# Performance work log

Hardware: AMD Instinct MI355X
Metric: run time of the kernel (lower is better)

The kernel has to match this reference:

```python
import jax, jax.numpy as jnp
import numpy as np

N_NODES = 50000
NEG_SLOPE = 0.2


def gat_conv(x, src, dst, W, att_src, att_dst, bias, concat):
    # x: [N, F_in], W: [H*D, F_in], att_*: [H, D], bias: [H*D] or [D]
    N = x.shape[0]
    H, D = att_src.shape
    h = (x @ W.T).reshape(N, H, D)                      # [N, H, D]
    a_src = jnp.einsum('nhd,hd->nh', h, att_src)        # [N, H]
    a_dst = jnp.einsum('nhd,hd->nh', h, att_dst)        # [N, H]
    e = jax.nn.leaky_relu(a_src[src] + a_dst[dst], NEG_SLOPE)  # [E, H]
    # softmax over incoming edges of each destination node
    m = jax.ops.segment_max(e, dst, num_segments=N)     # [N, H]
    ex = jnp.exp(e - m[dst])
    denom = jax.ops.segment_sum(ex, dst, num_segments=N)
    alpha = ex / denom[dst]                             # [E, H]
    msg = alpha[:, :, None] * h[src]                    # [E, H, D]
    out = jax.ops.segment_sum(msg, dst, num_segments=N) # [N, H, D]
    out = out.reshape(N, H * D) if concat else out.mean(axis=1)
    return out + bias


def setup_inputs() -> dict:
    key = jax.random.key(0)
    ks = jax.random.split(key, 10)
    nfeat, nhid, nclass, heads = 256, 128, 40, 4
    d1 = nhid // heads  # 32
    E = 800000
    x = jax.random.normal(ks[0], (N_NODES, nfeat), dtype=jnp.float32)
    edge_index = jax.random.randint(ks[1], (2, E), 0, N_NODES, dtype=jnp.int64)
    s = 0.1
    W1 = jax.random.normal(ks[2], (heads * d1, nfeat), dtype=jnp.float32) * s
    att_src1 = jax.random.normal(ks[3], (heads, d1), dtype=jnp.float32) * s
    att_dst1 = jax.random.normal(ks[4], (heads, d1), dtype=jnp.float32) * s
    b1 = jnp.zeros((heads * d1,), dtype=jnp.float32)
    W2 = jax.random.normal(ks[5], (nclass, nhid), dtype=jnp.float32) * s
    att_src2 = jax.random.normal(ks[6], (1, nclass), dtype=jnp.float32) * s
    att_dst2 = jax.random.normal(ks[7], (1, nclass), dtype=jnp.float32) * s
    b2 = jnp.zeros((nclass,), dtype=jnp.float32)
    return {"x": x, "edge_index": edge_index, "W1": W1, "att_src1": att_src1,
            "att_dst1": att_dst1, "b1": b1, "W2": W2, "att_src2": att_src2,
            "att_dst2": att_dst2, "b2": b2}


def reference(x, edge_index, W1, att_src1, att_dst1, b1, W2, att_src2, att_dst2, b2):
    # PyG GATConv adds self-loops by default
    loops = jnp.arange(N_NODES, dtype=edge_index.dtype)
    src = jnp.concatenate([edge_index[0], loops])
    dst = jnp.concatenate([edge_index[1], loops])
    h = gat_conv(x, src, dst, W1, att_src1, att_dst1, b1, concat=True)
    h = jax.nn.relu(h)
    # dropout is identity in eval mode
    out = gat_conv(h, src, dst, W2, att_src2, att_dst2, b2, concat=True)
    return out
```

## Files before the change

kernel.cpp:

```cpp
#include <hip/hip_runtime.h>
#include <hip/hip_bf16.h>
#include <cstdint>
#include <cstddef>

#define N_NODES 50000
#define NEG_SLOPE 0.2f
#define NB 196
#define BIN_CHUNK 8192
#define SLICE_MAX 14336

typedef float floatx4 __attribute__((ext_vector_type(4)));
typedef short shortx8 __attribute__((ext_vector_type(8)));

__device__ __forceinline__ unsigned short f2b(float f) {
    union { float f; unsigned u; } v; v.f = f;
    unsigned u = v.u;
    return (unsigned short)((u + 0x7FFFu + ((u >> 16) & 1u)) >> 16);
}
__device__ __forceinline__ float b2f(unsigned short b) {
    union { unsigned u; float f; } v; v.u = ((unsigned)b) << 16;
    return v.f;
}

__global__ __launch_bounds__(256) void bucket_hist_kernel(
    const int* __restrict__ ei, int E0, int E, int* __restrict__ bhist) {
    __shared__ int h[NB];
    int t = threadIdx.x;
    for (int i = t; i < NB; i += 256) h[i] = 0;
    __syncthreads();
    int base = blockIdx.x * BIN_CHUNK;
    int end = min(base + BIN_CHUNK, E);
    for (int e = base + t; e < end; e += 256) {
        int d = (e < E0) ? ei[E0 + e] : (e - E0);
        atomicAdd(&h[d >> 8], 1);
    }
    __syncthreads();
    for (int i = t; i < NB; i += 256)
        if (h[i]) atomicAdd(&bhist[i], h[i]);
}

__global__ __launch_bounds__(256) void bucket_scan_kernel(
    const int* __restrict__ bhist, int* __restrict__ bbase,
    int* __restrict__ bcursor, int* __restrict__ rowptr, int E) {
    __shared__ int buf[256];
    int t = threadIdx.x;
    int v = (t < NB) ? bhist[t] : 0;
    int x = v;
    for (int off = 1; off < 256; off <<= 1) {
        buf[t] = x; __syncthreads();
        int y = (t >= off) ? buf[t - off] : 0;
        __syncthreads();
        x += y;
    }
    if (t < NB) {
        bbase[t] = x - v;
        bcursor[t] = x - v;
    }
    if (t == NB - 1) bbase[NB] = x;
    if (t == 0) rowptr[N_NODES] = E;
}

__global__ __launch_bounds__(256) void bin_kernel(
    const int* __restrict__ ei, int E0, int E,
    int* __restrict__ bcursor, unsigned int* __restrict__ ebuf) {
    __shared__ int h[NB];
    __shared__ int gbase[NB];
    int t = threadIdx.x;
    for (int i = t; i < NB; i += 256) h[i] = 0;
    __syncthreads();
    int base = blockIdx.x * BIN_CHUNK;
    int end = min(base + BIN_CHUNK, E);
    for (int e = base + t; e < end; e += 256) {
        int d = (e < E0) ? ei[E0 + e] : (e - E0);
        atomicAdd(&h[d >> 8], 1);
    }
    __syncthreads();
    for (int i = t; i < NB; i += 256) {
        int c = h[i];
        gbase[i] = c ? atomicAdd(&bcursor[i], c) : 0;
        h[i] = 0;
    }
    __syncthreads();
    for (int e = base + t; e < end; e += 256) {
        int s, d;
        if (e < E0) { s = ei[e]; d = ei[E0 + e]; }
        else        { s = e - E0; d = e - E0; }
        int b = d >> 8;
        int off = atomicAdd(&h[b], 1);
        ebuf[gbase[b] + off] = (unsigned)s | ((unsigned)(d & 255) << 16);
    }
}

__global__ __launch_bounds__(256) void build_kernel(
    const unsigned int* __restrict__ ebuf, const int* __restrict__ bbase,
    int* __restrict__ rowptr, int* __restrict__ csr_src) {
    __shared__ int h[256];
    __shared__ int lrp[257];
    __shared__ int stag[SLICE_MAX];
    int b = blockIdx.x, t = threadIdx.x;
    int e0 = bbase[b], e1 = bbase[b + 1];
    int cnt = e1 - e0;
    int n0 = b << 8;
    h[t] = 0;
    __syncthreads();
    for (int i = t; i < cnt; i += 256)
        atomicAdd(&h[ebuf[e0 + i] >> 16], 1);
    __syncthreads();
    int v = h[t], x = v;
    __shared__ int buf[256];
    for (int off = 1; off < 256; off <<= 1) {
        buf[t] = x; __syncthreads();
        int y = (t >= off) ? buf[t - off] : 0;
        __syncthreads();
        x += y;
    }
    lrp[t] = x - v;
    if (t == 255) lrp[256] = x;
    h[t] = 0;
    __syncthreads();
    int n = n0 + t;
    if (n < N_NODES) rowptr[n] = e0 + lrp[t];
    for (int i = t; i < cnt; i += 256) {
        unsigned int v2 = ebuf[e0 + i];
        int dloc = v2 >> 16;
        int off = atomicAdd(&h[dloc], 1);
        stag[lrp[dloc] + off] = (int)(v2 & 0xFFFFu);
    }
    __syncthreads();
    for (int i = t; i < cnt; i += 256) csr_src[e0 + i] = stag[i];
}

template <int BM, int BN, int NREAL, int KK, typename InT>
__global__ __launch_bounds__(256) void gemm_bf16_kernel(
    const InT* __restrict__ A, const float* __restrict__ B,
    unsigned short* __restrict__ Cb, int M) {
    const int BK = 64, LDK = 72;
    const int NT = BN / 16;
    __shared__ unsigned short As[BM * LDK];
    __shared__ unsigned short Bs[BN * LDK];
    const int t = threadIdx.x;
    const int wave = t >> 6, lane = t & 63;
    const int lrow = lane & 15, lkg = lane >> 4;
    const int bm = blockIdx.x * BM;

    floatx4 acc[NT] = {};

    for (int k0 = 0; k0 < KK; k0 += BK) {
        __syncthreads();
        if constexpr (sizeof(InT) == 4) {
            for (int i = t; i < BM * 16; i += 256) {
                int r = i >> 4, c4 = (i & 15) << 2;
                int gr = bm + r;
                float4 v = make_float4(0.f, 0.f, 0.f, 0.f);
                if (gr < M) v = *(const float4*)&A[(size_t)gr * KK + k0 + c4];
                int o = r * LDK + c4;
                As[o] = f2b(v.x); As[o + 1] = f2b(v.y);
                As[o + 2] = f2b(v.z); As[o + 3] = f2b(v.w);
            }
        } else {
            for (int i = t; i < BM * 8; i += 256) {
                int r = i >> 3, c8 = (i & 7) << 3;
                int gr = bm + r;
                shortx8 v = {};
                if (gr < M) v = *(const shortx8*)&A[(size_t)gr * KK + k0 + c8];
                *(shortx8*)&As[r * LDK + c8] = v;
            }
        }
        for (int i = t; i < BN * 16; i += 256) {
            int r = i >> 4, c4 = (i & 15) << 2;
            float4 v = make_float4(0.f, 0.f, 0.f, 0.f);
            if (r < NREAL) v = *(const float4*)&B[(size_t)r * KK + k0 + c4];
            int o = r * LDK + c4;
            Bs[o] = f2b(v.x); Bs[o + 1] = f2b(v.y);
            Bs[o + 2] = f2b(v.z); Bs[o + 3] = f2b(v.w);
        }
        __syncthreads();

        for (int ks = 0; ks < BK; ks += 32) {
            int kc = ks + lkg * 8;
            int row = wave * 16 + lrow;
            shortx8 a = *(const shortx8*)&As[row * LDK + kc];
#pragma unroll
            for (int nt = 0; nt < NT; nt++) {
                shortx8 b = *(const shortx8*)&Bs[(nt * 16 + lrow) * LDK + kc];
                acc[nt] = __builtin_amdgcn_mfma_f32_16x16x32_bf16(a, b, acc[nt], 0, 0, 0);
            }
        }
    }
#pragma unroll
    for (int nt = 0; nt < NT; nt++)
#pragma unroll
        for (int r = 0; r < 4; r++) {
            int row = bm + wave * 16 + lkg * 4 + r;
            int col = nt * 16 + lrow;
            if (row < M && col < NREAL)
                Cb[(size_t)row * NREAL + col] = f2b(acc[nt][r]);
        }
}

__global__ void att1_kernel(const unsigned short* __restrict__ h1b,
                            const float* __restrict__ att_src,
                            const float* __restrict__ att_dst,
                            float* __restrict__ a_src, float* __restrict__ a_dst,
                            int N) {
    int i = blockIdx.x * blockDim.x + threadIdx.x;
    if (i >= N * 4) return;
    int h = i & 3;
    const ushort4* hp = (const ushort4*)(h1b + (size_t)i * 32);
    const float4* as = (const float4*)(att_src + h * 32);
    const float4* ad = (const float4*)(att_dst + h * 32);
    float ssum = 0.f, dsum = 0.f;
#pragma unroll
    for (int j = 0; j < 8; j++) {
        ushort4 hv = hp[j];
        float4 av = as[j], dv = ad[j];
        float x0 = b2f(hv.x), x1 = b2f(hv.y), x2 = b2f(hv.z), x3 = b2f(hv.w);
        ssum += x0 * av.x + x1 * av.y + x2 * av.z + x3 * av.w;
        dsum += x0 * dv.x + x1 * dv.y + x2 * dv.z + x3 * dv.w;
    }
    a_src[i] = ssum;
    a_dst[i] = dsum;
}

__global__ void att2_kernel(const unsigned short* __restrict__ h2b,
                            const float* __restrict__ att_src,
                            const float* __restrict__ att_dst,
                            float* __restrict__ a_src, float* __restrict__ a_dst,
                            int N) {
    int n = blockIdx.x * blockDim.x + threadIdx.x;
    if (n >= N) return;
    const ushort4* hp = (const ushort4*)(h2b + (size_t)n * 40);
    const float4* as = (const float4*)att_src;
    const float4* ad = (const float4*)att_dst;
    float ssum = 0.f, dsum = 0.f;
#pragma unroll
    for (int j = 0; j < 10; j++) {
        ushort4 hv = hp[j];
        float4 av = as[j], dv = ad[j];
        float x0 = b2f(hv.x), x1 = b2f(hv.y), x2 = b2f(hv.z), x3 = b2f(hv.w);
        ssum += x0 * av.x + x1 * av.y + x2 * av.z + x3 * av.w;
        dsum += x0 * dv.x + x1 * dv.y + x2 * dv.z + x3 * dv.w;
    }
    a_src[n] = ssum;
    a_dst[n] = dsum;
}

__global__ __launch_bounds__(256) void agg1_kernel(
    const unsigned short* __restrict__ h1b, const float* __restrict__ a_src,
    const float* __restrict__ a_dst, const int* __restrict__ rowptr,
    const int* __restrict__ csr_src, const float* __restrict__ b1,
    unsigned short* __restrict__ zb, int N) {
    int wave = threadIdx.x >> 6, lane = threadIdx.x & 63;
    int n = blockIdx.x * 4 + wave;
    if (n >= N) return;
    int half = lane >> 5, pos = lane & 31, head = pos >> 3;
    float adn = a_dst[n * 4 + (lane & 3)];
    int beg = rowptr[n], deg = rowptr[n + 1] - beg;

    floatx4 acc = {0.f, 0.f, 0.f, 0.f};
    float den = 0.f;
    for (int c0 = 0; c0 < deg; c0 += 16) {
        int idx = c0 + (lane >> 2);
        int s_e = (idx < deg) ? csr_src[beg + idx] : 0;
        float l = a_src[(s_e << 2) + (lane & 3)] + adn;
        l = l > 0.f ? l : NEG_SLOPE * l;
        float w_e = __expf(l);
        int cnt = min(16, deg - c0);
#pragma unroll
        for (int e = 0; e < 16; e += 2) {
            int el = e + half;
            int s = __shfl(s_e, el << 2);
            float w = __shfl(w_e, (el << 2) + head);
            if (el < cnt) {
                ushort4 v = *(const ushort4*)&h1b[(size_t)s * 128 + pos * 4];
                den += w;
                acc.x += w * b2f(v.x); acc.y += w * b2f(v.y);
                acc.z += w * b2f(v.z); acc.w += w * b2f(v.w);
            }
        }
    }
    acc.x += __shfl_xor(acc.x, 32);
    acc.y += __shfl_xor(acc.y, 32);
    acc.z += __shfl_xor(acc.z, 32);
    acc.w += __shfl_xor(acc.w, 32);
    den   += __shfl_xor(den, 32);
    if (half == 0) {
        float inv = 1.f / den;
        float4 bb = *(const float4*)&b1[pos * 4];
        float o0 = fmaxf(acc.x * inv + bb.x, 0.f);
        float o1 = fmaxf(acc.y * inv + bb.y, 0.f);
        float o2 = fmaxf(acc.z * inv + bb.z, 0.f);
        float o3 = fmaxf(acc.w * inv + bb.w, 0.f);
        ushort4 r;
        r.x = f2b(o0); r.y = f2b(o1); r.z = f2b(o2); r.w = f2b(o3);
        *(ushort4*)&zb[(size_t)n * 128 + pos * 4] = r;
    }
}

__global__ __launch_bounds__(256) void agg2_kernel(
    const unsigned short* __restrict__ h2b, const float* __restrict__ a_src,
    const float* __restrict__ a_dst, const int* __restrict__ rowptr,
    const int* __restrict__ csr_src, const float* __restrict__ b2,
    float* __restrict__ out, int N) {
    int wave = threadIdx.x >> 6, lane = threadIdx.x & 63;
    int n = blockIdx.x * 4 + wave;
    if (n >= N) return;
    int half = lane >> 5, pos = lane & 31;
    float adn = a_dst[n];
    int beg = rowptr[n], deg = rowptr[n + 1] - beg;

    float2 acc = {0.f, 0.f};
    float den = 0.f;
    for (int c0 = 0; c0 < deg; c0 += 32) {
        int idx = c0 + lane;
        int s_e = (idx < deg) ? csr_src[beg + idx] : 0;
        float l = a_src[s_e] + adn;
        l = l > 0.f ? l : NEG_SLOPE * l;
        float w_e = __expf(l);
        int cnt = min(32, deg - c0);
#pragma unroll
        for (int e = 0; e < 32; e += 2) {
            int el = e + half;
            int s = __shfl(s_e, el);
            float w = __shfl(w_e, el);
            if (el < cnt) {
                den += w;
                if (pos < 20) {
                    ushort2 v = *(const ushort2*)&h2b[(size_t)s * 40 + pos * 2];
                    acc.x += w * b2f(v.x);
                    acc.y += w * b2f(v.y);
                }
            }
        }
    }
    acc.x += __shfl_xor(acc.x, 32);
    acc.y += __shfl_xor(acc.y, 32);
    den   += __shfl_xor(den, 32);
    if (half == 0 && pos < 20) {
        float inv = 1.f / den;
        float2 bb = *(const float2*)&b2[pos * 2];
        float2 o;
        o.x = acc.x * inv + bb.x;
        o.y = acc.y * inv + bb.y;
        *(float2*)&out[(size_t)n * 40 + pos * 2] = o;
    }
}

extern "C" void kernel_launch(void* const* d_in, const int* in_sizes, int n_in,
                              void* d_out, int out_size, void* d_ws, size_t ws_size,
                              hipStream_t stream) {
    const float* x        = (const float*)d_in[0];
    const int*   ei       = (const int*)d_in[1];
    const float* W1       = (const float*)d_in[2];
    const float* att_src1 = (const float*)d_in[3];
    const float* att_dst1 = (const float*)d_in[4];
    const float* b1       = (const float*)d_in[5];
    const float* W2       = (const float*)d_in[6];
    const float* att_src2 = (const float*)d_in[7];
    const float* att_dst2 = (const float*)d_in[8];
    const float* b2       = (const float*)d_in[9];
    float* out = (float*)d_out;

    const int N  = N_NODES;
    const int E0 = in_sizes[1] / 2;
    const int E  = E0 + N;
    const int NBLK = (E + BIN_CHUNK - 1) / BIN_CHUNK;

    char* ws = (char*)d_ws;
    unsigned short* h1b = (unsigned short*)(ws + 0);
    unsigned short* zb  = (unsigned short*)(ws + 12800000);
    unsigned short* h2b = (unsigned short*)(ws + 25600000);
    float* a_src1 = (float*)(ws + 29600000);
    float* a_dst1 = (float*)(ws + 30400000);
    float* a_src2 = (float*)(ws + 31200000);
    float* a_dst2 = (float*)(ws + 31400000);
    int*   rowptr = (int*)(ws + 31600000);
    int*   bhist  = (int*)(ws + 31800192);
    int*   bbase  = (int*)(ws + 31801088);
    int*   bcursor= (int*)(ws + 31801984);
    unsigned int* ebuf = (unsigned int*)(ws + 31802880);
    int*   csr_src= (int*)(ws + 35202880);

    hipMemsetAsync(bhist, 0, NB * sizeof(int), stream);

    bucket_hist_kernel<<<NBLK, 256, 0, stream>>>(ei, E0, E, bhist);
    bucket_scan_kernel<<<1, 256, 0, stream>>>(bhist, bbase, bcursor, rowptr, E);
    bin_kernel<<<NBLK, 256, 0, stream>>>(ei, E0, E, bcursor, ebuf);
    build_kernel<<<NB, 256, 0, stream>>>(ebuf, bbase, rowptr, csr_src);

    gemm_bf16_kernel<64, 128, 128, 256, float>
        <<<(N + 63) / 64, 256, 0, stream>>>(x, W1, h1b, N);
    att1_kernel<<<(N * 4 + 255) / 256, 256, 0, stream>>>(h1b, att_src1, att_dst1, a_src1, a_dst1, N);
    agg1_kernel<<<(N + 3) / 4, 256, 0, stream>>>(h1b, a_src1, a_dst1, rowptr, csr_src, b1, zb, N);

    gemm_bf16_kernel<64, 48, 40, 128, unsigned short>
        <<<(N + 63) / 64, 256, 0, stream>>>(zb, W2, h2b, N);
    att2_kernel<<<(N + 255) / 256, 256, 0, stream>>>(h2b, att_src2, att_dst2, a_src2, a_dst2, N);
    agg2_kernel<<<(N + 3) / 4, 256, 0, stream>>>(h2b, a_src2, a_dst2, rowptr, csr_src, b2, out, N);
}
```

Measured before the change: 267.4 us.

## Precompute per-edge attention weights in separate kernels and keep layer-2 features in fp32

The build kernel now also emits a per-edge destination array. Two new edge-parallel kernels compute the exp(leaky_relu) attention weights for every CSR edge ahead of aggregation, so the aggregation kernels only load precomputed weights instead of gathering a_src and computing exp per node. Layer-2 features are now stored as fp32 instead of bf16, which adds gather bandwidth in agg2 but improves precision. The cost is two extra launches plus writing and re-reading the edge-weight arrays (16 bytes per edge for layer 1).

```diff
diff --git a/kernel.cpp b/kernel.cpp
--- a/kernel.cpp
+++ b/kernel.cpp
@@ -93,10 +93,11 @@
 
 __global__ __launch_bounds__(256) void build_kernel(
     const unsigned int* __restrict__ ebuf, const int* __restrict__ bbase,
-    int* __restrict__ rowptr, int* __restrict__ csr_src) {
+    int* __restrict__ rowptr, int* __restrict__ csr_src,
+    unsigned short* __restrict__ csr_dst) {
     __shared__ int h[256];
     __shared__ int lrp[257];
-    __shared__ int stag[SLICE_MAX];
+    __shared__ unsigned int stag[SLICE_MAX];
     int b = blockIdx.x, t = threadIdx.x;
     int e0 = bbase[b], e1 = bbase[b + 1];
     int cnt = e1 - e0;
@@ -124,16 +125,50 @@
         unsigned int v2 = ebuf[e0 + i];
         int dloc = v2 >> 16;
         int off = atomicAdd(&h[dloc], 1);
-        stag[lrp[dloc] + off] = (int)(v2 & 0xFFFFu);
-    }
-    __syncthreads();
-    for (int i = t; i < cnt; i += 256) csr_src[e0 + i] = stag[i];
-}
-
-template <int BM, int BN, int NREAL, int KK, typename InT>
+        stag[lrp[dloc] + off] = v2;
+    }
+    __syncthreads();
+    for (int i = t; i < cnt; i += 256) {
+        unsigned int v2 = stag[i];
+        csr_src[e0 + i] = (int)(v2 & 0xFFFFu);
+        csr_dst[e0 + i] = (unsigned short)(n0 + (v2 >> 16));
+    }
+}
+
+__global__ __launch_bounds__(256) void edge_w1_kernel(
+    const int* __restrict__ csr_src, const unsigned short* __restrict__ csr_dst,
+    const float* __restrict__ a_src, const float* __restrict__ a_dst,
+    float* __restrict__ ew, int E) {
+    int e = blockIdx.x * blockDim.x + threadIdx.x;
+    if (e >= E) return;
+    int s = csr_src[e];
+    int d = csr_dst[e];
+    float4 as = *(const float4*)&a_src[s << 2];
+    float4 ad = *(const float4*)&a_dst[d << 2];
+    float4 w;
+    float l;
+    l = as.x + ad.x; l = l > 0.f ? l : NEG_SLOPE * l; w.x = __expf(l);
+    l = as.y + ad.y; l = l > 0.f ? l : NEG_SLOPE * l; w.y = __expf(l);
+    l = as.z + ad.z; l = l > 0.f ? l : NEG_SLOPE * l; w.z = __expf(l);
+    l = as.w + ad.w; l = l > 0.f ? l : NEG_SLOPE * l; w.w = __expf(l);
+    *(float4*)&ew[(size_t)e << 2] = w;
+}
+
+__global__ __launch_bounds__(256) void edge_w2_kernel(
+    const int* __restrict__ csr_src, const unsigned short* __restrict__ csr_dst,
+    const float* __restrict__ a_src, const float* __restrict__ a_dst,
+    float* __restrict__ ew, int E) {
+    int e = blockIdx.x * blockDim.x + threadIdx.x;
+    if (e >= E) return;
+    float l = a_src[csr_src[e]] + a_dst[csr_dst[e]];
+    l = l > 0.f ? l : NEG_SLOPE * l;
+    ew[e] = __expf(l);
+}
+
+template <int BM, int BN, int NREAL, int KK, typename InT, typename OutT>
 __global__ __launch_bounds__(256) void gemm_bf16_kernel(
     const InT* __restrict__ A, const float* __restrict__ B,
-    unsigned short* __restrict__ Cb, int M) {
+    OutT* __restrict__ C, int M) {
     const int BK = 64, LDK = 72;
     const int NT = BN / 16;
     __shared__ unsigned short As[BM * LDK];
@@ -193,8 +228,12 @@
         for (int r = 0; r < 4; r++) {
             int row = bm + wave * 16 + lkg * 4 + r;
             int col = nt * 16 + lrow;
-            if (row < M && col < NREAL)
-                Cb[(size_t)row * NREAL + col] = f2b(acc[nt][r]);
+            if (row < M && col < NREAL) {
+                if constexpr (sizeof(OutT) == 2)
+                    C[(size_t)row * NREAL + col] = f2b(acc[nt][r]);
+                else
+                    C[(size_t)row * NREAL + col] = acc[nt][r];
+            }
         }
 }
 
@@ -222,39 +261,36 @@
     a_dst[i] = dsum;
 }
 
-__global__ void att2_kernel(const unsigned short* __restrict__ h2b,
+__global__ void att2_kernel(const float* __restrict__ h2,
                             const float* __restrict__ att_src,
                             const float* __restrict__ att_dst,
                             float* __restrict__ a_src, float* __restrict__ a_dst,
                             int N) {
     int n = blockIdx.x * blockDim.x + threadIdx.x;
     if (n >= N) return;
-    const ushort4* hp = (const ushort4*)(h2b + (size_t)n * 40);
+    const float4* hp = (const float4*)(h2 + (size_t)n * 40);
     const float4* as = (const float4*)att_src;
     const float4* ad = (const float4*)att_dst;
     float ssum = 0.f, dsum = 0.f;
 #pragma unroll
     for (int j = 0; j < 10; j++) {
-        ushort4 hv = hp[j];
+        float4 hv = hp[j];
         float4 av = as[j], dv = ad[j];
-        float x0 = b2f(hv.x), x1 = b2f(hv.y), x2 = b2f(hv.z), x3 = b2f(hv.w);
-        ssum += x0 * av.x + x1 * av.y + x2 * av.z + x3 * av.w;
-        dsum += x0 * dv.x + x1 * dv.y + x2 * dv.z + x3 * dv.w;
+        ssum += hv.x * av.x + hv.y * av.y + hv.z * av.z + hv.w * av.w;
+        dsum += hv.x * dv.x + hv.y * dv.y + hv.z * dv.z + hv.w * dv.w;
     }
     a_src[n] = ssum;
     a_dst[n] = dsum;
 }
 
 __global__ __launch_bounds__(256) void agg1_kernel(
-    const unsigned short* __restrict__ h1b, const float* __restrict__ a_src,
-    const float* __restrict__ a_dst, const int* __restrict__ rowptr,
-    const int* __restrict__ csr_src, const float* __restrict__ b1,
-    unsigned short* __restrict__ zb, int N) {
+    const unsigned short* __restrict__ h1b, const float* __restrict__ ew,
+    const int* __restrict__ rowptr, const int* __restrict__ csr_src,
+    const float* __restrict__ b1, unsigned short* __restrict__ zb, int N) {
     int wave = threadIdx.x >> 6, lane = threadIdx.x & 63;
     int n = blockIdx.x * 4 + wave;
     if (n >= N) return;
     int half = lane >> 5, pos = lane & 31, head = pos >> 3;
-    float adn = a_dst[n * 4 + (lane & 3)];
     int beg = rowptr[n], deg = rowptr[n + 1] - beg;
 
     floatx4 acc = {0.f, 0.f, 0.f, 0.f};
@@ -262,9 +298,7 @@
     for (int c0 = 0; c0 < deg; c0 += 16) {
         int idx = c0 + (lane >> 2);
         int s_e = (idx < deg) ? csr_src[beg + idx] : 0;
-        float l = a_src[(s_e << 2) + (lane & 3)] + adn;
-        l = l > 0.f ? l : NEG_SLOPE * l;
-        float w_e = __expf(l);
+        float w_e = (idx < deg) ? ew[((size_t)(beg + c0) << 2) + lane] : 0.f;
         int cnt = min(16, deg - c0);
 #pragma unroll
         for (int e = 0; e < 16; e += 2) {
@@ -298,25 +332,24 @@
 }
 
 __global__ __launch_bounds__(256) void agg2_kernel(
-    const unsigned short* __restrict__ h2b, const float* __restrict__ a_src,
-    const float* __restrict__ a_dst, const int* __restrict__ rowptr,
-    const int* __restrict__ csr_src, const float* __restrict__ b2,
-    float* __restrict__ out, int N) {
+    const float* __restrict__ h2, const float* __restrict__ ew,
+    const int* __restrict__ rowptr, const int* __restrict__ csr_src,
+    const float* __restrict__ b2, float* __restrict__ out, int N) {
     int wave = threadIdx.x >> 6, lane = threadIdx.x & 63;
     int n = blockIdx.x * 4 + wave;
     if (n >= N) return;
     int half = lane >> 5, pos = lane & 31;
-    float adn = a_dst[n];
     int beg = rowptr[n], deg = rowptr[n + 1] - beg;
 
     float2 acc = {0.f, 0.f};
     float den = 0.f;
     for (int c0 = 0; c0 < deg; c0 += 32) {
         int idx = c0 + lane;
-        int s_e = (idx < deg) ? csr_src[beg + idx] : 0;
-        float l = a_src[s_e] + adn;
-        l = l > 0.f ? l : NEG_SLOPE * l;
-        float w_e = __expf(l);
+        int s_e = 0; float w_e = 0.f;
+        if (lane < 32 && idx < deg) {
+            s_e = csr_src[beg + idx];
+            w_e = ew[beg + idx];
+        }
         int cnt = min(32, deg - c0);
 #pragma unroll
         for (int e = 0; e < 32; e += 2) {
@@ -326,9 +359,9 @@
             if (el < cnt) {
                 den += w;
                 if (pos < 20) {
-                    ushort2 v = *(const ushort2*)&h2b[(size_t)s * 40 + pos * 2];
-                    acc.x += w * b2f(v.x);
-                    acc.y += w * b2f(v.y);
+                    float2 v = *(const float2*)&h2[(size_t)s * 40 + pos * 2];
+                    acc.x += w * v.x;
+                    acc.y += w * v.y;
                 }
             }
         }
@@ -369,32 +402,37 @@
     char* ws = (char*)d_ws;
     unsigned short* h1b = (unsigned short*)(ws + 0);
     unsigned short* zb  = (unsigned short*)(ws + 12800000);
-    unsigned short* h2b = (unsigned short*)(ws + 25600000);
-    float* a_src1 = (float*)(ws + 29600000);
-    float* a_dst1 = (float*)(ws + 30400000);
-    float* a_src2 = (float*)(ws + 31200000);
-    float* a_dst2 = (float*)(ws + 31400000);
-    int*   rowptr = (int*)(ws + 31600000);
-    int*   bhist  = (int*)(ws + 31800192);
-    int*   bbase  = (int*)(ws + 31801088);
-    int*   bcursor= (int*)(ws + 31801984);
-    unsigned int* ebuf = (unsigned int*)(ws + 31802880);
-    int*   csr_src= (int*)(ws + 35202880);
+    float*          h2  = (float*)(ws + 25600000);
+    float* a_src1 = (float*)(ws + 33600000);
+    float* a_dst1 = (float*)(ws + 34400000);
+    float* a_src2 = (float*)(ws + 35200000);
+    float* a_dst2 = (float*)(ws + 35400000);
+    int*   rowptr = (int*)(ws + 35600000);
+    int*   bhist  = (int*)(ws + 35800192);
+    int*   bbase  = (int*)(ws + 35801088);
+    int*   bcursor= (int*)(ws + 35801984);
+    unsigned int* ebuf = (unsigned int*)(ws + 35802880);
+    int*   csr_src= (int*)(ws + 39202880);
+    unsigned short* csr_dst = (unsigned short*)(ws + 42602880);
+    float* ew1    = (float*)(ws + 44302880);
+    float* ew2    = (float*)(ws + 57902880);
 
     hipMemsetAsync(bhist, 0, NB * sizeof(int), stream);
 
     bucket_hist_kernel<<<NBLK, 256, 0, stream>>>(ei, E0, E, bhist);
     bucket_scan_kernel<<<1, 256, 0, stream>>>(bhist, bbase, bcursor, rowptr, E);
     bin_kernel<<<NBLK, 256, 0, stream>>>(ei, E0, E, bcursor, ebuf);
-    build_kernel<<<NB, 256, 0, stream>>>(ebuf, bbase, rowptr, csr_src);
-
-    gemm_bf16_kernel<64, 128, 128, 256, float>
+    build_kernel<<<NB, 256, 0, stream>>>(ebuf, bbase, rowptr, csr_src, csr_dst);
+
+    gemm_bf16_kernel<64, 128, 128, 256, float, unsigned short>
         <<<(N + 63) / 64, 256, 0, stream>>>(x, W1, h1b, N);
     att1_kernel<<<(N * 4 + 255) / 256, 256, 0, stream>>>(h1b, att_src1, att_dst1, a_src1, a_dst1, N);
-    agg1_kernel<<<(N + 3) / 4, 256, 0, stream>>>(h1b, a_src1, a_dst1, rowptr, csr_src, b1, zb, N);
-
-    gemm_bf16_kernel<64, 48, 40, 128, unsigned short>
-        <<<(N + 63) / 64, 256, 0, stream>>>(zb, W2, h2b, N);
-    att2_kernel<<<(N + 255) / 256, 256, 0, stream>>>(h2b, att_src2, att_dst2, a_src2, a_dst2, N);
-    agg2_kernel<<<(N + 3) / 4, 256, 0, stream>>>(h2b, a_src2, a_dst2, rowptr, csr_src, b2, out, N);
-}
+    edge_w1_kernel<<<(E + 255) / 256, 256, 0, stream>>>(csr_src, csr_dst, a_src1, a_dst1, ew1, E);
+    agg1_kernel<<<(N + 3) / 4, 256, 0, stream>>>(h1b, ew1, rowptr, csr_src, b1, zb, N);
+
+    gemm_bf16_kernel<64, 48, 40, 128, unsigned short, float>
+        <<<(N + 63) / 64, 256, 0, stream>>>(zb, W2, h2, N);
+    att2_kernel<<<(N + 255) / 256, 256, 0, stream>>>(h2, att_src2, att_dst2, a_src2, a_dst2, N);
+    edge_w2_kernel<<<(E + 255) / 256, 256, 0, stream>>>(csr_src, csr_dst, a_src2, a_dst2, ew2, E);
+    agg2_kernel<<<(N + 3) / 4, 256, 0, stream>>>(h2, ew2, rowptr, csr_src, b2, out, N);
+}
```

Result: slower. 281.1 us (+5.1%).
